# Kernel optimization log

Measured on AMD Instinct MI355X. Metric: run time of the kernel, lower is better.

## Reference

```python
import jax, jax.numpy as jnp
import numpy as np

EMBED_DIM = 512
NUM_HEADS = 8
HEAD_DIM = EMBED_DIM // NUM_HEADS
EDGE_DIM = 16
B, N = 2, 2048


def setup_inputs() -> dict:
    key = jax.random.key(0)
    ks = jax.random.split(key, 16)
    s = 1.0 / np.sqrt(EMBED_DIM)
    inp = {
        "x": jax.random.normal(ks[0], (B, N, EMBED_DIM), dtype=jnp.float32),
        "adjacency": jax.random.uniform(ks[1], (B, N, N), dtype=jnp.float32),
        # torch.nn.Linear stores weight as (out, in); we keep that convention
        "Wq": jax.random.uniform(ks[2], (EMBED_DIM, EMBED_DIM), minval=-s, maxval=s),
        "bq": jax.random.uniform(ks[3], (EMBED_DIM,), minval=-s, maxval=s),
        "Wk": jax.random.uniform(ks[4], (EMBED_DIM, EMBED_DIM), minval=-s, maxval=s),
        "bk": jax.random.uniform(ks[5], (EMBED_DIM,), minval=-s, maxval=s),
        "Wv": jax.random.uniform(ks[6], (EMBED_DIM, EMBED_DIM), minval=-s, maxval=s),
        "bv": jax.random.uniform(ks[7], (EMBED_DIM,), minval=-s, maxval=s),
        "Wo": jax.random.uniform(ks[8], (EMBED_DIM, EMBED_DIM), minval=-s, maxval=s),
        "bo": jax.random.uniform(ks[9], (EMBED_DIM,), minval=-s, maxval=s),
        # edge MLP: Linear(1 -> edge_dim) then Linear(edge_dim -> num_heads)
        "We1": jax.random.uniform(ks[10], (EDGE_DIM, 1), minval=-1.0, maxval=1.0),
        "be1": jax.random.uniform(ks[11], (EDGE_DIM,), minval=-1.0, maxval=1.0),
        "We2": jax.random.uniform(ks[12], (NUM_HEADS, EDGE_DIM), minval=-0.25, maxval=0.25),
        "be2": jax.random.uniform(ks[13], (NUM_HEADS,), minval=-0.25, maxval=0.25),
        "edge_bias": jnp.zeros((NUM_HEADS,), dtype=jnp.float32),
    }
    return inp


def reference(x, adjacency, Wq, bq, Wk, bk, Wv, bv, Wo, bo, We1, be1, We2, be2, edge_bias):
    b, n, _ = x.shape
    scale = HEAD_DIM ** (-0.5)

    def split_heads(t):  # (b, n, E) -> (b, H, n, d)
        return t.reshape(b, n, NUM_HEADS, HEAD_DIM).transpose(0, 2, 1, 3)

    q = split_heads(x @ Wq.T + bq)
    k = split_heads(x @ Wk.T + bk)
    v = split_heads(x @ Wv.T + bv)

    # (b, H, n, n)
    attn_scores = jnp.einsum('bhid,bhjd->bhij', q, k) * scale

    # edge MLP applied pointwise to each adjacency entry: 1 -> edge_dim -> num_heads
    # hidden: (b, n, n, edge_dim)
    hidden = jax.nn.relu(adjacency[..., None] * We1[:, 0] + be1)
    edge_attn = jnp.einsum('bijE,hE->bhij', hidden, We2) + be2[None, :, None, None]

    boost = adjacency[:, None, :, :] * edge_bias[None, :, None, None]
    attn_scores = attn_scores + edge_attn + boost

    attn_probs = jax.nn.softmax(attn_scores, axis=-1)
    out = jnp.einsum('bhij,bhjd->bhid', attn_probs, v)
    out = out.transpose(0, 2, 1, 3).reshape(b, n, EMBED_DIM)
    out = out @ Wo.T + bo
    return out
```

## Files before the change

### kernel.cpp

```cpp
#include <hip/hip_runtime.h>
#include <stdint.h>


#define SEQ 2048
#define EMB 512
#define NH  8
#define HD  64
#define NB  2
#define L2E 1.4426950408889634f

typedef unsigned int   u32;
typedef unsigned short u16;
typedef u32   u32x4  __attribute__((ext_vector_type(4)));
typedef float f32x4  __attribute__((ext_vector_type(4)));
typedef __bf16 bf16x8 __attribute__((ext_vector_type(8)));

#define MFMA16(a, b, c) __builtin_amdgcn_mfma_f32_16x16x32_bf16((a), (b), (c), 0, 0, 0)

static __device__ __forceinline__ u16 f2bf(float f) {
  return __builtin_bit_cast(u16, (__bf16)f);
}
static __device__ __forceinline__ u32 pack2(float a, float b) {
  return (u32)f2bf(a) | ((u32)f2bf(b) << 16);
}
static __device__ __forceinline__ bf16x8 ldfrag(const u16* p) {
  return __builtin_bit_cast(bf16x8, *(const u32x4*)p);
}
static __device__ __forceinline__ void glds16(const u16* g, u16* l) {
  __builtin_amdgcn_global_load_lds(
      (const __attribute__((address_space(1))) u32*)(const void*)g,
      (__attribute__((address_space(3))) u32*)(void*)l, 16, 0, 0);
}


__global__ void prep_kernel(const float* __restrict__ x,
                            const float* __restrict__ Wq, const float* __restrict__ Wk,
                            const float* __restrict__ Wv, const float* __restrict__ Wo,
                            const float* __restrict__ We1, const float* __restrict__ be1,
                            const float* __restrict__ We2, const float* __restrict__ be2,
                            const float* __restrict__ ebias,
                            u16* __restrict__ xb, u16* __restrict__ wqkv,
                            u16* __restrict__ wob, float* __restrict__ co) {
  const int blk = blockIdx.x, tid = threadIdx.x;
  if (blk < 2048) {
    int i = (blk * 256 + tid) * 4;
    float4 v = *(const float4*)(x + i);
    *(uint2*)(xb + i) = make_uint2(pack2(v.x, v.y), pack2(v.z, v.w));
  } else if (blk < 3072) {
    int i = ((blk - 2048) * 256 + tid) * 4;
    int m = i >> 18;
    int off = i & 262143;
    const float* src = (m == 0) ? Wq : ((m == 1) ? Wk : ((m == 2) ? Wv : Wo));
    u16* dst = (m < 3) ? (wqkv + (size_t)m * 262144) : wob;
    float4 v = *(const float4*)(src + off);
    *(uint2*)(dst + off) = make_uint2(pack2(v.x, v.y), pack2(v.z, v.w));
  } else {
    const int e = tid & 15, h = tid >> 4;
    if (tid < 128) {
      co[49 + e * 8 + h] = 0.0f;
      if (h == 0) { co[17 + e] = 0.0f; co[33 + e] = 0.0f; }
    }
    __syncthreads();
    if (tid < 128) {
      float w1 = We1[e], b1 = be1[e], w2 = We2[h * 16 + e];
      float u0 = b1, u1 = w1 + b1;
      bool on  = (u0 >= 0.0f) && (u1 >= 0.0f);
      bool off = (u0 <= 0.0f) && (u1 <= 0.0f);
      bool crossing = (!on) && (!off);
      float ca = on ? (w2 * b1) : (crossing ? 0.5f * w2 * b1 : 0.0f);
      float cb = on ? (w2 * w1) : (crossing ? 0.5f * w2 * w1 : 0.0f);
      #pragma unroll
      for (int d = 1; d < 16; d <<= 1) { ca += __shfl_xor(ca, d); cb += __shfl_xor(cb, d); }
      if (e == 0) { co[h] = (be2[h] + ca) * L2E; co[8 + h] = (ebias[h] + cb) * L2E; }
      unsigned long long msk = __ballot(crossing);
      int midx = __popcll(msk & 0xFFFFull & ((1ull << e) - 1ull));
      int mcnt = __popcll(msk & 0xFFFFull);
      if (crossing) {
        co[49 + midx * 8 + h] = 0.5f * w2 * L2E;
        if (h == 0) { co[17 + midx] = w1; co[33 + midx] = b1; }
      }
      if (tid == 0) ((int*)co)[16] = mcnt;
    }
  }
}

#define LDA 40
__global__ __launch_bounds__(256) void gemm_qkv_kernel(
    const u16* __restrict__ A, const u16* __restrict__ Bm,
    const float* __restrict__ bq, const float* __restrict__ bk, const float* __restrict__ bv,
    u16* __restrict__ qh, u16* __restrict__ ksw, u16* __restrict__ vsw)
{
  __shared__ u16 sm[64 * LDA + 128 * LDA];
  u16* As = sm;
  u16* Bs = sm + 64 * LDA;
  const int tid = threadIdx.x;
  const int lane = tid & 63, w = tid >> 6;
  const int q = lane >> 4, l15 = lane & 15;
  const int m0 = blockIdx.y * 64;
  const int n0 = blockIdx.x * 128;

  f32x4 acc[4][2];
  f32x4 zero = {0.f, 0.f, 0.f, 0.f};
  #pragma unroll
  for (int i = 0; i < 4; i++) { acc[i][0] = zero; acc[i][1] = zero; }

  const bool isA = tid < 128;
  const int arow_ = tid >> 1, ahalf = tid & 1;
  const int brow = tid - 128;
  const u16* ga = A  + (size_t)(m0 + arow_) * EMB + ahalf * 16;
  const u16* gb = Bm + (size_t)(n0 + brow) * EMB;
  u16* la = &As[arow_ * LDA + ahalf * 16];
  u16* lb = &Bs[brow * LDA];

  u32x4 p0, p1, p2, p3;
  if (isA) {
    p0 = *(const u32x4*)(ga); p1 = *(const u32x4*)(ga + 8); ga += 32;
  } else {
    p0 = *(const u32x4*)(gb);      p1 = *(const u32x4*)(gb + 8);
    p2 = *(const u32x4*)(gb + 16); p3 = *(const u32x4*)(gb + 24); gb += 32;
  }

  for (int k0 = 0; k0 < EMB; k0 += 32) {
    __syncthreads();
    if (isA) { *(u32x4*)(la) = p0; *(u32x4*)(la + 8) = p1; }
    else {
      *(u32x4*)(lb)      = p0; *(u32x4*)(lb + 8)  = p1;
      *(u32x4*)(lb + 16) = p2; *(u32x4*)(lb + 24) = p3;
    }
    __syncthreads();
    if (k0 + 32 < EMB) {
      if (isA) { p0 = *(const u32x4*)(ga); p1 = *(const u32x4*)(ga + 8); ga += 32; }
      else {
        p0 = *(const u32x4*)(gb);      p1 = *(const u32x4*)(gb + 8);
        p2 = *(const u32x4*)(gb + 16); p3 = *(const u32x4*)(gb + 24); gb += 32;
      }
    }
    bf16x8 af[4], bfr[2];
    #pragma unroll
    for (int mi = 0; mi < 4; mi++)
      af[mi] = ldfrag(&As[(mi*16 + l15) * LDA + q*8]);
    #pragma unroll
    for (int ni = 0; ni < 2; ni++)
      bfr[ni] = ldfrag(&Bs[(w*32 + ni*16 + l15) * LDA + q*8]);
    #pragma unroll
    for (int mi = 0; mi < 4; mi++)
      #pragma unroll
      for (int ni = 0; ni < 2; ni++)
        acc[mi][ni] = MFMA16(af[mi], bfr[ni], acc[mi][ni]);
  }

  const int mat = n0 >> 9;
  const float* bias = (mat == 0) ? bq : ((mat == 1) ? bk : bv);
  const float mul = (mat == 0) ? 0.125f * L2E : 1.0f;
  const int b_ = m0 >> 11;
  const int nbase = m0 & 2047;

  #pragma unroll
  for (int p = 0; p < 2; p++) {
    __syncthreads();
    if ((w >> 1) == p) {
      #pragma unroll
      for (int ni = 0; ni < 2; ni++) {
        const int dd = (w & 1) * 32 + ni * 16 + l15;
        const float bsv = bias[(n0 & 511) + (w * 32 + ni * 16 + l15)];
        #pragma unroll
        for (int mi = 0; mi < 4; mi++) {
          #pragma unroll
          for (int r = 0; r < 4; r++) {
            const int nr = mi * 16 + q * 4 + r;
            const float val = (acc[mi][ni][r] + bsv) * mul;
            int idx;
            if (mat == 0)      idx = nr * 64 + dd;
            else if (mat == 1) idx = (nr >> 4) * 1024 + ((dd >> 5) << 9)
                                   + ((((dd >> 3) & 3) * 16 + (nr & 15)) << 3) + (dd & 7);
            else               idx = ((dd >> 4) << 10) + (((nr >> 5) & 1) << 9)
                                   + ((((nr >> 3) & 3) * 16 + (dd & 15)) << 3) + (nr & 7);
            sm[idx] = f2bf(val);
          }
        }
      }
    }
    __syncthreads();
    const int hh = ((n0 & 511) >> 6) + p;
    u16* gdst;
    if (mat == 0)      gdst = qh  + ((size_t)(b_ * NH + hh) * SEQ + nbase) * HD;
    else if (mat == 1) gdst = ksw + (size_t)(b_ * NH + hh) * 131072 + (nbase >> 4) * 1024;
    else               gdst = vsw + (size_t)(b_ * NH + hh) * 131072 + (nbase >> 6) * 4096;
    *(u32x4*)(gdst + tid * 16)     = *(const u32x4*)(sm + tid * 16);
    *(u32x4*)(gdst + tid * 16 + 8) = *(const u32x4*)(sm + tid * 16 + 8);
  }
}

__global__ __launch_bounds__(256) void gemm_out_kernel(
    const u16* __restrict__ A, const u16* __restrict__ Bm,
    const float* __restrict__ bo, float* __restrict__ out)
{
  __shared__ u16 As[64 * LDA];
  __shared__ u16 Bs[64 * LDA];
  const int tid = threadIdx.x;
  const int lane = tid & 63, w = tid >> 6;
  const int q = lane >> 4, l15 = lane & 15;
  const int m0 = blockIdx.y * 64;
  const int n0 = blockIdx.x * 64;

  f32x4 acc[4];
  f32x4 zero = {0.f, 0.f, 0.f, 0.f};
  #pragma unroll
  for (int i = 0; i < 4; i++) acc[i] = zero;

  const bool isA = tid < 128;
  const int row = isA ? (tid >> 1) : ((tid - 128) >> 1);
  const int half = tid & 1;
  const u16* g = (isA ? A + (size_t)(m0 + row) * EMB : Bm + (size_t)(n0 + row) * EMB)
               + half * 16;
  u16* l = (isA ? &As[row * LDA] : &Bs[row * LDA]) + half * 16;

  u32x4 p0 = *(const u32x4*)(g);
  u32x4 p1 = *(const u32x4*)(g + 8);
  g += 32;

  for (int k0 = 0; k0 < EMB; k0 += 32) {
    __syncthreads();
    *(u32x4*)(l) = p0; *(u32x4*)(l + 8) = p1;
    __syncthreads();
    if (k0 + 32 < EMB) {
      p0 = *(const u32x4*)(g); p1 = *(const u32x4*)(g + 8); g += 32;
    }
    bf16x8 af[4], bfr;
    #pragma unroll
    for (int mi = 0; mi < 4; mi++)
      af[mi] = ldfrag(&As[(mi*16 + l15) * LDA + q*8]);
    bfr = ldfrag(&Bs[(w*16 + l15) * LDA + q*8]);
    #pragma unroll
    for (int mi = 0; mi < 4; mi++)
      acc[mi] = MFMA16(af[mi], bfr, acc[mi]);
  }

  int col = n0 + w*16 + l15;
  float bsv = bo[col];
  #pragma unroll
  for (int mi = 0; mi < 4; mi++) {
    int rowb = m0 + mi*16 + q*4;
    #pragma unroll
    for (int r = 0; r < 4; r++)
      out[(size_t)(rowb + r) * EMB + col] = acc[mi][r] + bsv;
  }
}

template<int MT>
struct FlashCtx {
  const u16 *kgp, *vgp;
  const float* arow;
  bf16x8 qf0, qf1;
  float Ah, Bh;
  float ctr[MT], dtr[MT], wtr[MT];
  int lane, w, q, l15, pxor;
};

template<int MT>
static __device__ __forceinline__ void flash_stageV(const FlashCtx<MT>& c,
                                                    u16* Vb, int it) {
  const int o = c.w * 1024 + c.lane * 8;
  const u16* vg = c.vgp + it * 4096;
  glds16(vg + o,       Vb + o);
  glds16(vg + o + 512, Vb + o + 512);
}

template<int MT>
static __device__ __forceinline__ void flash_iter(
    const FlashCtx<MT>& c, int it, int tend, u16* Vb, u16* nVb,
    u16* psw, float4* avc, float4* avn, f32x4* O, float& lsum)
{
  asm volatile("s_waitcnt vmcnt(4)" ::: "memory");
  __builtin_amdgcn_s_barrier();
  __builtin_amdgcn_sched_barrier(0);

  const u16* kg = c.kgp + it * 4096 + c.lane * 8;
  bf16x8 kf[8];
  #pragma unroll
  for (int jt = 0; jt < 4; jt++) {
    kf[2*jt]   = ldfrag(kg + jt * 1024);
    kf[2*jt+1] = ldfrag(kg + jt * 1024 + 512);
  }
  __builtin_amdgcn_sched_barrier(0);
  if (it + 1 < tend) flash_stageV(c, nVb, it + 1);
  const int nx = (it + 1 < tend) ? it + 1 : tend - 1;
  #pragma unroll
  for (int jt = 0; jt < 4; jt++)
    avn[jt] = *(const float4*)(c.arow + nx * 64 + jt * 16);
  __builtin_amdgcn_sched_barrier(0);

  f32x4 zero = {0.f, 0.f, 0.f, 0.f};
  const int lo = c.lane * 8;

  f32x4 S[4];
  #pragma unroll
  for (int jt = 0; jt < 4; jt++) {
    f32x4 s = MFMA16(kf[2*jt], c.qf0, zero);
    S[jt] = MFMA16(kf[2*jt+1], c.qf1, s);
  }

  #pragma unroll
  for (int half = 0; half < 2; half++) {
    #pragma unroll
    for (int jj = 0; jj < 2; jj++) {
      const int jt = half * 2 + jj;
      float p[4];
      #pragma unroll
      for (int r = 0; r < 4; r++) {
        float a = ((const float*)&avc[jt])[r];
        float e = fmaf(a, c.Bh, c.Ah);
        #pragma unroll
        for (int t = 0; t < MT; t++)
          e = fmaf(fabsf(fmaf(a, c.ctr[t], c.dtr[t])), c.wtr[t], e);
        p[r] = __builtin_amdgcn_exp2f(S[jt][r] + e);
        lsum += p[r];
      }
      *(uint2*)(psw + ((c.l15 * 64 + jt * 16 + c.q * 4) ^ c.pxor)) =
          make_uint2(pack2(p[0], p[1]), pack2(p[2], p[3]));
    }
    bf16x8 pf = ldfrag(psw + ((c.l15 * 64 + half * 32 + c.q * 8) ^ c.pxor));
    #pragma unroll
    for (int dt = 0; dt < 4; dt++) {
      bf16x8 vf = ldfrag(Vb + dt * 1024 + half * 512 + lo);
      O[dt] = MFMA16(vf, pf, O[dt]);
    }
  }
}

template<int MT>
__device__ __forceinline__ void flash_body(
    u16* Vb0, u16* Vb1, u16* Pb,
    const u16* __restrict__ qh, const u16* __restrict__ ksw, const u16* __restrict__ vsw,
    const float* __restrict__ adj, const float* __restrict__ coeff,
    u16* __restrict__ om0, u16* __restrict__ om1, float* __restrict__ lsp)
{
  const int tid = threadIdx.x, lane = tid & 63, w = tid >> 6;
  const int q = lane >> 4, l15 = lane & 15;
  const int bidf = blockIdx.x + 32 * (blockIdx.y + 8 * blockIdx.z);
  const int swz  = (bidf & 7) * 128 + (bidf >> 3);
  const int i0 = (swz & 31) * 64;
  const int h  = (swz >> 5) & 7;
  const int zz = swz >> 8;
  const int b = zz >> 1, jh = zz & 1;
  const int t0 = jh * 16, tend = t0 + 16;
  const int bh = b * NH + h;
  const int iw = i0 + w * 16;

  FlashCtx<MT> c;
  c.lane = lane; c.w = w; c.q = q; c.l15 = l15;
  c.pxor = (l15 & 7) << 3;
  c.Ah = coeff[h]; c.Bh = coeff[8 + h];
  #pragma unroll
  for (int t = 0; t < MT; t++) {
    c.ctr[t] = coeff[17 + t];
    c.dtr[t] = coeff[33 + t];
    c.wtr[t] = coeff[49 + t * 8 + h];
  }
  const u16* qrow = qh + ((size_t)bh * SEQ + iw + l15) * HD;
  c.qf0 = ldfrag(qrow + q * 8);
  c.qf1 = ldfrag(qrow + 32 + q * 8);
  c.kgp = ksw + (size_t)bh * 131072;
  c.vgp = vsw + (size_t)bh * 131072;
  c.arow = adj + ((size_t)b * SEQ + iw + l15) * SEQ + q * 4;

  f32x4 O[4];
  f32x4 zero = {0.f, 0.f, 0.f, 0.f};
  #pragma unroll
  for (int dt = 0; dt < 4; dt++) O[dt] = zero;
  float lsum = 0.0f;

  u16* psw = Pb + w * 1024;

  flash_stageV(c, Vb0, t0);
  float4 avA[4], avB[4];
  #pragma unroll
  for (int jt = 0; jt < 4; jt++)
    avA[jt] = *(const float4*)(c.arow + t0 * 64 + jt * 16);

  #pragma unroll 1
  for (int it2 = t0; it2 < tend; it2 += 2) {
    flash_iter(c, it2,     tend, Vb0, Vb1, psw, avA, avB, O, lsum);
    flash_iter(c, it2 + 1, tend, Vb1, Vb0, psw, avB, avA, O, lsum);
  }

  lsum += __shfl_xor(lsum, 16);
  lsum += __shfl_xor(lsum, 32);
  if (lane < 16)
    lsp[(size_t)jh * 32768 + (size_t)bh * SEQ + iw + l15] = lsum;

  u16* orow = (jh ? om1 : om0)
            + ((size_t)b * SEQ + iw + l15) * EMB + h * HD + q * 4;
  #pragma unroll
  for (int dt = 0; dt < 4; dt++)
    *(uint2*)(orow + dt * 16) = make_uint2(pack2(O[dt][0], O[dt][1]),
                                           pack2(O[dt][2], O[dt][3]));
}

__global__ __launch_bounds__(256, 4) void flash_kernel(
    const u16* __restrict__ qh, const u16* __restrict__ ksw, const u16* __restrict__ vsw,
    const float* __restrict__ adj, const float* __restrict__ coeff,
    u16* __restrict__ om0, u16* __restrict__ om1, float* __restrict__ lsp)
{
  __shared__ __align__(16) u16 Vb[2][4096];
  __shared__ __align__(16) u16 Pb[4096];
  const int mt = ((const int*)coeff)[16];
  if (mt <= 4)
    flash_body<4>(Vb[0], Vb[1], Pb, qh, ksw, vsw, adj, coeff, om0, om1, lsp);
  else if (mt <= 8)
    flash_body<8>(Vb[0], Vb[1], Pb, qh, ksw, vsw, adj, coeff, om0, om1, lsp);
  else
    flash_body<16>(Vb[0], Vb[1], Pb, qh, ksw, vsw, adj, coeff, om0, om1, lsp);
}

__global__ __launch_bounds__(256) void combine_kernel(
    u16* __restrict__ om0, const u16* __restrict__ om1,
    const float* __restrict__ lsp)
{
  const int g = blockIdx.x * 256 + threadIdx.x;
  const int idx = g * 4;
  const int row = idx >> 9;
  const int h = (idx >> 6) & 7;
  const int li = ((row >> 11) * NH + h) * SEQ + (row & 2047);
  const float rl = 1.0f / (lsp[li] + lsp[32768 + li]);
  uint2 a = *(const uint2*)(om0 + idx);
  uint2 d = *(const uint2*)(om1 + idx);
  const float o0 = __builtin_bit_cast(float, a.x << 16)
                 + __builtin_bit_cast(float, d.x << 16);
  const float o1 = __builtin_bit_cast(float, a.x & 0xffff0000u)
                 + __builtin_bit_cast(float, d.x & 0xffff0000u);
  const float o2 = __builtin_bit_cast(float, a.y << 16)
                 + __builtin_bit_cast(float, d.y << 16);
  const float o3 = __builtin_bit_cast(float, a.y & 0xffff0000u)
                 + __builtin_bit_cast(float, d.y & 0xffff0000u);
  *(uint2*)(om0 + idx) = make_uint2(pack2(o0 * rl, o1 * rl),
                                    pack2(o2 * rl, o3 * rl));
}

extern "C" void kernel_launch(void* const* d_in, const int* in_sizes, int n_in,
                              void* d_out, int out_size, void* d_ws, size_t ws_size,
                              hipStream_t stream) {
  const float* x     = (const float*)d_in[0];
  const float* adj   = (const float*)d_in[1];
  const float* Wq    = (const float*)d_in[2];
  const float* bq    = (const float*)d_in[3];
  const float* Wk    = (const float*)d_in[4];
  const float* bk    = (const float*)d_in[5];
  const float* Wv    = (const float*)d_in[6];
  const float* bv    = (const float*)d_in[7];
  const float* Wo    = (const float*)d_in[8];
  const float* bo    = (const float*)d_in[9];
  const float* We1   = (const float*)d_in[10];
  const float* be1   = (const float*)d_in[11];
  const float* We2   = (const float*)d_in[12];
  const float* be2   = (const float*)d_in[13];
  const float* ebias = (const float*)d_in[14];
  float* out = (float*)d_out;

  char* ws = (char*)d_ws;
  u16*   xb   = (u16*)(ws + 0);
  u16*   wqkv = (u16*)(ws + 4194304);
  u16*   wob  = (u16*)(ws + 5767168);
  u16*   qh   = (u16*)(ws + 6291456);
  u16*   ksw  = (u16*)(ws + 10485760);
  u16*   vsw  = (u16*)(ws + 14680064);
  u16*   om0  = (u16*)(ws + 18874368);
  float* co   = (float*)(ws + 23068672);
  u16*   om1  = xb;
  float* lsp  = (float*)wqkv;
  if (ws_size < 23069696) return;

  prep_kernel<<<3073, 256, 0, stream>>>(x, Wq, Wk, Wv, Wo, We1, be1, We2, be2, ebias,
                                        xb, wqkv, wob, co);
  gemm_qkv_kernel<<<dim3(12, 64), 256, 0, stream>>>(xb, wqkv, bq, bk, bv, qh, ksw, vsw);
  flash_kernel<<<dim3(32, NH, NB * 2), 256, 0, stream>>>(qh, ksw, vsw, adj, co,
                                                         om0, om1, lsp);
  combine_kernel<<<2048, 256, 0, stream>>>(om0, om1, lsp);
  gemm_out_kernel<<<dim3(8, 64), 256, 0, stream>>>(om0, wob, bo, out);
}
```

Measured before the change: 203.6 us.

## Load V fragments directly to registers and software-prefetch K/V in flash loop

Removes the LDS double-buffered V staging (global_load_lds plus per-iteration waitcnt and barrier). K and V fragments are now held in registers and the next tile is prefetched from global memory right after the current tile's MFMAs are issued. The block-index swizzle is dropped in favour of a plain grid mapping, and a periodic barrier keeps waves loosely synchronised. Occupancy is lowered from 4 to 3 blocks per SM to make room for the extra register fragments, which risks less latency hiding and worse L2 locality without the swizzle.

Result: slower. 240.7 us (+18.2%).

```diff
diff --git a/kernel.cpp b/kernel.cpp
--- a/kernel.cpp
+++ b/kernel.cpp
@@ -25,11 +25,6 @@
 }
 static __device__ __forceinline__ bf16x8 ldfrag(const u16* p) {
   return __builtin_bit_cast(bf16x8, *(const u32x4*)p);
-}
-static __device__ __forceinline__ void glds16(const u16* g, u16* l) {
-  __builtin_amdgcn_global_load_lds(
-      (const __attribute__((address_space(1))) u32*)(const void*)g,
-      (__attribute__((address_space(3))) u32*)(void*)l, 16, 0, 0);
 }
 
 
@@ -258,46 +253,31 @@
 };
 
 template<int MT>
-static __device__ __forceinline__ void flash_stageV(const FlashCtx<MT>& c,
-                                                    u16* Vb, int it) {
-  const int o = c.w * 1024 + c.lane * 8;
-  const u16* vg = c.vgp + it * 4096;
-  glds16(vg + o,       Vb + o);
-  glds16(vg + o + 512, Vb + o + 512);
-}
-
-template<int MT>
 static __device__ __forceinline__ void flash_iter(
-    const FlashCtx<MT>& c, int it, int tend, u16* Vb, u16* nVb,
+    const FlashCtx<MT>& c, int it, int tend, bf16x8* kf, bf16x8* vf,
     u16* psw, float4* avc, float4* avn, f32x4* O, float& lsum)
 {
-  asm volatile("s_waitcnt vmcnt(4)" ::: "memory");
-  __builtin_amdgcn_s_barrier();
-  __builtin_amdgcn_sched_barrier(0);
-
-  const u16* kg = c.kgp + it * 4096 + c.lane * 8;
-  bf16x8 kf[8];
-  #pragma unroll
-  for (int jt = 0; jt < 4; jt++) {
-    kf[2*jt]   = ldfrag(kg + jt * 1024);
-    kf[2*jt+1] = ldfrag(kg + jt * 1024 + 512);
-  }
-  __builtin_amdgcn_sched_barrier(0);
-  if (it + 1 < tend) flash_stageV(c, nVb, it + 1);
   const int nx = (it + 1 < tend) ? it + 1 : tend - 1;
   #pragma unroll
   for (int jt = 0; jt < 4; jt++)
     avn[jt] = *(const float4*)(c.arow + nx * 64 + jt * 16);
-  __builtin_amdgcn_sched_barrier(0);
 
   f32x4 zero = {0.f, 0.f, 0.f, 0.f};
-  const int lo = c.lane * 8;
 
   f32x4 S[4];
   #pragma unroll
   for (int jt = 0; jt < 4; jt++) {
     f32x4 s = MFMA16(kf[2*jt], c.qf0, zero);
     S[jt] = MFMA16(kf[2*jt+1], c.qf1, s);
+  }
+
+  if (it + 1 < tend) {
+    const u16* kg = c.kgp + (it + 1) * 4096 + c.lane * 8;
+    #pragma unroll
+    for (int jt = 0; jt < 4; jt++) {
+      kf[2*jt]   = ldfrag(kg + jt * 1024);
+      kf[2*jt+1] = ldfrag(kg + jt * 1024 + 512);
+    }
   }
 
   #pragma unroll
@@ -321,28 +301,32 @@
     }
     bf16x8 pf = ldfrag(psw + ((c.l15 * 64 + half * 32 + c.q * 8) ^ c.pxor));
     #pragma unroll
+    for (int dt = 0; dt < 4; dt++)
+      O[dt] = MFMA16(vf[dt * 2 + half], pf, O[dt]);
+  }
+
+  if (it + 1 < tend) {
+    const u16* vg = c.vgp + (it + 1) * 4096 + c.lane * 8;
+    #pragma unroll
     for (int dt = 0; dt < 4; dt++) {
-      bf16x8 vf = ldfrag(Vb + dt * 1024 + half * 512 + lo);
-      O[dt] = MFMA16(vf, pf, O[dt]);
+      vf[dt*2]   = ldfrag(vg + dt * 1024);
+      vf[dt*2+1] = ldfrag(vg + dt * 1024 + 512);
     }
   }
 }
 
 template<int MT>
 __device__ __forceinline__ void flash_body(
-    u16* Vb0, u16* Vb1, u16* Pb,
+    u16* Pb,
     const u16* __restrict__ qh, const u16* __restrict__ ksw, const u16* __restrict__ vsw,
     const float* __restrict__ adj, const float* __restrict__ coeff,
     u16* __restrict__ om0, u16* __restrict__ om1, float* __restrict__ lsp)
 {
   const int tid = threadIdx.x, lane = tid & 63, w = tid >> 6;
   const int q = lane >> 4, l15 = lane & 15;
-  const int bidf = blockIdx.x + 32 * (blockIdx.y + 8 * blockIdx.z);
-  const int swz  = (bidf & 7) * 128 + (bidf >> 3);
-  const int i0 = (swz & 31) * 64;
-  const int h  = (swz >> 5) & 7;
-  const int zz = swz >> 8;
-  const int b = zz >> 1, jh = zz & 1;
+  const int i0 = blockIdx.x * 64;
+  const int h = blockIdx.y;
+  const int b = blockIdx.z >> 1, jh = blockIdx.z & 1;
   const int t0 = jh * 16, tend = t0 + 16;
   const int bh = b * NH + h;
   const int iw = i0 + w * 16;
@@ -372,7 +356,18 @@
 
   u16* psw = Pb + w * 1024;
 
-  flash_stageV(c, Vb0, t0);
+  bf16x8 kf[8], vf[8];
+  {
+    const u16* kg = c.kgp + t0 * 4096 + lane * 8;
+    const u16* vg = c.vgp + t0 * 4096 + lane * 8;
+    #pragma unroll
+    for (int jt = 0; jt < 4; jt++) {
+      kf[2*jt]   = ldfrag(kg + jt * 1024);
+      kf[2*jt+1] = ldfrag(kg + jt * 1024 + 512);
+      vf[2*jt]   = ldfrag(vg + jt * 1024);
+      vf[2*jt+1] = ldfrag(vg + jt * 1024 + 512);
+    }
+  }
   float4 avA[4], avB[4];
   #pragma unroll
   for (int jt = 0; jt < 4; jt++)
@@ -380,8 +375,9 @@
 
   #pragma unroll 1
   for (int it2 = t0; it2 < tend; it2 += 2) {
-    flash_iter(c, it2,     tend, Vb0, Vb1, psw, avA, avB, O, lsum);
-    flash_iter(c, it2 + 1, tend, Vb1, Vb0, psw, avB, avA, O, lsum);
+    flash_iter(c, it2,     tend, kf, vf, psw, avA, avB, O, lsum);
+    flash_iter(c, it2 + 1, tend, kf, vf, psw, avB, avA, O, lsum);
+    if (it2 & 2) __builtin_amdgcn_s_barrier();
   }
 
   lsum += __shfl_xor(lsum, 16);
@@ -397,20 +393,19 @@
                                            pack2(O[dt][2], O[dt][3]));
 }
 
-__global__ __launch_bounds__(256, 4) void flash_kernel(
+__global__ __launch_bounds__(256, 3) void flash_kernel(
     const u16* __restrict__ qh, const u16* __restrict__ ksw, const u16* __restrict__ vsw,
     const float* __restrict__ adj, const float* __restrict__ coeff,
     u16* __restrict__ om0, u16* __restrict__ om1, float* __restrict__ lsp)
 {
-  __shared__ __align__(16) u16 Vb[2][4096];
   __shared__ __align__(16) u16 Pb[4096];
   const int mt = ((const int*)coeff)[16];
   if (mt <= 4)
-    flash_body<4>(Vb[0], Vb[1], Pb, qh, ksw, vsw, adj, coeff, om0, om1, lsp);
+    flash_body<4>(Pb, qh, ksw, vsw, adj, coeff, om0, om1, lsp);
   else if (mt <= 8)
-    flash_body<8>(Vb[0], Vb[1], Pb, qh, ksw, vsw, adj, coeff, om0, om1, lsp);
+    flash_body<8>(Pb, qh, ksw, vsw, adj, coeff, om0, om1, lsp);
   else
-    flash_body<16>(Vb[0], Vb[1], Pb, qh, ksw, vsw, adj, coeff, om0, om1, lsp);
+    flash_body<16>(Pb, qh, ksw, vsw, adj, coeff, om0, om1, lsp);
 }
 
 __global__ __launch_bounds__(256) void combine_kernel(
```
